# Optimization experiments

Hardware: AMD Instinct MI355X
Metric: run time of the kernel (lower is better)

Reference implementation:

```python
import jax, jax.numpy as jnp
import numpy as np

NEG_SLOPE = 0.2  # PyG GATConv default negative_slope


def gat_layer(x, edge_index, W, att_src, att_dst, bias):
    """GATConv with self-loops, concat heads. x:[N,F_in], W:[F_in,H*C]."""
    N = x.shape[0]
    H, C = att_src.shape
    loop = jnp.arange(N, dtype=edge_index.dtype)
    src = jnp.concatenate([edge_index[0], loop])  # [E+N]
    dst = jnp.concatenate([edge_index[1], loop])
    h = (x @ W).reshape(N, H, C)                  # [N,H,C]
    a_src = jnp.einsum('nhc,hc->nh', h, att_src)  # [N,H]
    a_dst = jnp.einsum('nhc,hc->nh', h, att_dst)
    e = a_src[src] + a_dst[dst]                   # [E+N,H]
    e = jnp.where(e > 0, e, NEG_SLOPE * e)        # leaky_relu
    # numerically-stable segment softmax over incoming edges of each dst node
    m = jax.ops.segment_max(e, dst, num_segments=N)           # [N,H]
    ex = jnp.exp(e - m[dst])
    denom = jax.ops.segment_sum(ex, dst, num_segments=N)      # [N,H]
    alpha = ex / (denom[dst] + 1e-16)                          # [E+N,H]
    out = jax.ops.segment_sum(h[src] * alpha[:, :, None], dst, num_segments=N)
    return out.reshape(N, H * C) + bias


def setup_inputs() -> dict:
    key = jax.random.key(0)
    ks = jax.random.split(key, 16)
    N, E, F_IN, HID, H, NCLS = 50000, 800000, 128, 64, 4, 40
    HC = H * HID
    s = 0.1
    return {
        'x': jax.random.normal(ks[0], (N, F_IN), jnp.float32),
        'edge_index': jax.random.randint(ks[1], (2, E), 0, N, jnp.int32),
        'W1': jax.random.normal(ks[2], (F_IN, HC), jnp.float32) * s,
        'att_src1': jax.random.normal(ks[3], (H, HID), jnp.float32) * s,
        'att_dst1': jax.random.normal(ks[4], (H, HID), jnp.float32) * s,
        'b1': jnp.zeros((HC,), jnp.float32),
        'W2': jax.random.normal(ks[5], (HC, HC), jnp.float32) * s,
        'att_src2': jax.random.normal(ks[6], (H, HID), jnp.float32) * s,
        'att_dst2': jax.random.normal(ks[7], (H, HID), jnp.float32) * s,
        'b2': jnp.zeros((HC,), jnp.float32),
        'fcW1': jax.random.normal(ks[8], (HC, HID), jnp.float32) * s,
        'fcb1': jnp.zeros((HID,), jnp.float32),
        'fcW2': jax.random.normal(ks[9], (HID, NCLS), jnp.float32) * s,
        'fcb2': jnp.zeros((NCLS,), jnp.float32),
    }


def reference(x, edge_index, W1, att_src1, att_dst1, b1,
              W2, att_src2, att_dst2, b2, fcW1, fcb1, fcW2, fcb2):
    h = gat_layer(x, edge_index, W1, att_src1, att_dst1, b1)
    h = jax.nn.elu(h)
    h = gat_layer(h, edge_index, W2, att_src2, att_dst2, b2)
    h = jax.nn.elu(h)
    h = jnp.maximum(h @ fcW1 + fcb1, 0.0)  # ReLU; dropout is identity in eval
    return h @ fcW2 + fcb2                 # [N, num_classes]
```

## Files before the change

kernel.cpp:

```cpp
#include <hip/hip_runtime.h>

typedef __attribute__((ext_vector_type(8))) _Float16 fp16x8;
typedef __attribute__((ext_vector_type(4))) float f32x4;
typedef __attribute__((ext_vector_type(4))) _Float16 h4;
typedef unsigned int u32;

__device__ __forceinline__ float lrelu(float x) { return x > 0.f ? x : 0.2f * x; }
__device__ __forceinline__ float elu(float x) { return x > 0.f ? x : __expf(x) - 1.f; }

__device__ __forceinline__ void gl2lds16(const void* g, void* l) {
    __builtin_amdgcn_global_load_lds((const __attribute__((address_space(1))) u32*)g,
                                     (__attribute__((address_space(3))) u32*)l, 16, 0, 0);
}

__device__ __forceinline__ void t16t_body(const float* __restrict__ W, _Float16* __restrict__ T,
                                          int N, int Nreal, int t) {
    int lane = t & 63, rem = t >> 6;
    int kk = rem & 1; rem >>= 1;
    int ncg = N / 16;
    int cg = rem % ncg, kc = rem / ncg;
    int k = kc * 64 + kk * 32 + (lane >> 4) * 8;
    int n = cg * 16 + (lane & 15);
    fp16x8 o;
#pragma unroll
    for (int j = 0; j < 8; ++j)
        o[j] = (n < Nreal) ? (_Float16)W[(size_t)(k + j) * Nreal + n] : (_Float16)0.f;
    *(fp16x8*)(T + (size_t)t * 8) = o;
}

__global__ __launch_bounds__(256) void k_prep(const float* __restrict__ W1, _Float16* __restrict__ W1T,
                                              const float* __restrict__ W2, _Float16* __restrict__ W2T,
                                              const float* __restrict__ fcW1, _Float16* __restrict__ fWT,
                                              const float* __restrict__ fcW2, _Float16* __restrict__ f2T,
                                              const int* __restrict__ dst, int* __restrict__ cnt) {
    int b = blockIdx.x, tid = threadIdx.x;
    if (b < 16)      t16t_body(W1, W1T, 256, 256, b * 256 + tid);
    else if (b < 48) t16t_body(W2, W2T, 256, 256, (b - 16) * 256 + tid);
    else if (b < 56) t16t_body(fcW1, fWT, 64, 64, (b - 48) * 256 + tid);
    else if (b < 58) t16t_body(fcW2, f2T, 64, 40, (b - 56) * 256 + tid);
    else             atomicAdd(&cnt[dst[(b - 58) * 256 + tid]], 1);
}

__global__ __launch_bounds__(256) void k_scan_a(const int* __restrict__ cnt, int* __restrict__ s,
                                                int* __restrict__ partial, int N) {
    __shared__ int sh[256];
    int t = threadIdx.x, gid = blockIdx.x * 256 + t;
    sh[t] = gid < N ? cnt[gid] : 0;
    __syncthreads();
    for (int off = 1; off < 256; off <<= 1) {
        int add = (t >= off) ? sh[t - off] : 0;
        __syncthreads();
        sh[t] += add;
        __syncthreads();
    }
    if (gid < N) s[gid] = sh[t];
    if (t == 255) partial[blockIdx.x] = sh[255];
}
__global__ __launch_bounds__(256) void k_scan_bc(const int* __restrict__ s, const int* __restrict__ partial,
                                                 const int* __restrict__ cnt, int* __restrict__ row_ptr,
                                                 int* __restrict__ cursor, int N) {
    __shared__ int red[256];
    int t = threadIdx.x, bid = blockIdx.x;
    int a = 0;
    for (int i = t; i < bid; i += 256) a += partial[i];
    red[t] = a;
    __syncthreads();
    for (int off = 128; off; off >>= 1) {
        if (t < off) red[t] += red[t + off];
        __syncthreads();
    }
    int base = red[0];
    int gid = bid * 256 + t;
    if (gid >= N) return;
    int val = s[gid] + base;
    row_ptr[gid + 1] = val;
    cursor[gid] = val - cnt[gid];
    if (gid == 0) row_ptr[0] = 0;
}

template<int KV, int NW, int ATT, int AFP32>
__device__ __forceinline__ void gemm_body(int bid,
              const _Float16* __restrict__ Ah, const float* __restrict__ Af,
              const _Float16* __restrict__ BT, _Float16* __restrict__ Chi,
              const float* __restrict__ att_s, const float* __restrict__ att_d,
              float* __restrict__ a_src, float* __restrict__ a_dst,
              int M, int Nc) {
    constexpr int NCG = NW / 16;
    constexpr int CHUNK = NW * 64;
    constexpr int FPW = (CHUNK / 512) / 4;
    __shared__ _Float16 Bs[CHUNK];
    const int m0 = bid * 64;
    const int tid = threadIdx.x;
    const int lane = tid & 63, wv = tid >> 6;
    const int r16 = lane & 15, quad = lane >> 4;
    const int arow = min(m0 + wv * 16 + r16, M - 1);

    f32x4 acc[NCG];
#pragma unroll
    for (int cg = 0; cg < NCG; ++cg) acc[cg] = (f32x4){0, 0, 0, 0};

    constexpr int NCH = KV / 64;
#pragma unroll
    for (int kc = 0; kc < NCH; ++kc) {
        if (kc) __syncthreads();
#pragma unroll
        for (int f = 0; f < FPW; ++f) {
            int fr = wv * FPW + f;
            gl2lds16(BT + (size_t)kc * CHUNK + fr * 512 + lane * 8, &Bs[fr * 512]);
        }
        fp16x8 ar[2];
        if (AFP32) {
            const float* Ap = Af + (size_t)arow * KV + kc * 64 + quad * 8;
#pragma unroll
            for (int kk = 0; kk < 2; ++kk) {
                float4 u0 = *(const float4*)(Ap + kk * 32);
                float4 u1 = *(const float4*)(Ap + kk * 32 + 4);
                fp16x8 h8;
                h8[0] = (_Float16)u0.x; h8[1] = (_Float16)u0.y;
                h8[2] = (_Float16)u0.z; h8[3] = (_Float16)u0.w;
                h8[4] = (_Float16)u1.x; h8[5] = (_Float16)u1.y;
                h8[6] = (_Float16)u1.z; h8[7] = (_Float16)u1.w;
                ar[kk] = h8;
            }
        } else {
            const _Float16* Ahp = Ah + (size_t)arow * KV + kc * 64 + quad * 8;
#pragma unroll
            for (int kk = 0; kk < 2; ++kk) ar[kk] = *(const fp16x8*)(Ahp + kk * 32);
        }
        __syncthreads();
#pragma unroll
        for (int kk = 0; kk < 2; ++kk) {
#pragma unroll
            for (int cg = 0; cg < NCG; ++cg) {
                fp16x8 bh = *(const fp16x8*)(&Bs[(cg * 2 + kk) * 512 + lane * 8]);
                acc[cg] = __builtin_amdgcn_mfma_f32_16x16x32_f16(ar[kk], bh, acc[cg], 0, 0, 0);
            }
        }
    }

    const int rbase = m0 + wv * 16 + quad * 4;

    if (ATT) {
#pragma unroll
        for (int hq = 0; hq < 4; ++hq) {
            float as[4], ad[4];
#pragma unroll
            for (int cg = 0; cg < 4; ++cg) {
                as[cg] = att_s[hq * 64 + cg * 16 + r16];
                ad[cg] = att_d[hq * 64 + cg * 16 + r16];
            }
#pragma unroll
            for (int i = 0; i < 4; ++i) {
                float ps = acc[hq * 4 + 0][i] * as[0] + acc[hq * 4 + 1][i] * as[1]
                         + acc[hq * 4 + 2][i] * as[2] + acc[hq * 4 + 3][i] * as[3];
                float pd = acc[hq * 4 + 0][i] * ad[0] + acc[hq * 4 + 1][i] * ad[1]
                         + acc[hq * 4 + 2][i] * ad[2] + acc[hq * 4 + 3][i] * ad[3];
#pragma unroll
                for (int d = 1; d < 16; d <<= 1) {
                    ps += __shfl_xor(ps, d);
                    pd += __shfl_xor(pd, d);
                }
                int r = rbase + i;
                if (r16 == 0 && r < M) {
                    a_src[(size_t)r * 4 + hq] = ps;
                    a_dst[(size_t)r * 4 + hq] = pd;
                }
            }
        }
    }

#pragma unroll
    for (int cg = 0; cg < NCG; ++cg) {
        int c = cg * 16 + r16;
        if (c >= Nc) continue;
#pragma unroll
        for (int i = 0; i < 4; ++i) {
            int r = rbase + i;
            if (r < M) Chi[(size_t)r * Nc + c] = (_Float16)acc[cg][i];
        }
    }
}

__global__ __launch_bounds__(256, 4)
void k_work1(const float* __restrict__ x, const _Float16* __restrict__ W1T,
             _Float16* __restrict__ h,
             const float* __restrict__ att_s, const float* __restrict__ att_d,
             float* __restrict__ a_src, float* __restrict__ a_dst,
             const int* __restrict__ src, const int* __restrict__ dst,
             int* __restrict__ cursor, int* __restrict__ csr,
             int M, int E, int RB) {
    if ((int)blockIdx.x >= RB) {
        int e = (blockIdx.x - RB) * 256 + threadIdx.x;
        if (e < E) {
            int d = dst[e];
            int pos = atomicAdd(&cursor[d], 1);
            csr[pos] = src[e];
        }
        return;
    }
    gemm_body<128, 256, 1, 1>(blockIdx.x, nullptr, x, W1T, h, att_s, att_d, a_src, a_dst, M, 256);
}

__global__ __launch_bounds__(256, 4)
void k_gemm2(const _Float16* __restrict__ Ah, const _Float16* __restrict__ BT,
             _Float16* __restrict__ h,
             const float* __restrict__ att_s, const float* __restrict__ att_d,
             float* __restrict__ a_src, float* __restrict__ a_dst, int M) {
    gemm_body<256, 256, 1, 0>(blockIdx.x, Ah, nullptr, BT, h, att_s, att_d, a_src, a_dst, M, 256);
}

__global__ __launch_bounds__(256, 4)
void k_fc(const _Float16* __restrict__ Ah, const _Float16* __restrict__ BT1,
          const _Float16* __restrict__ BT2, const float* __restrict__ b1,
          const float* __restrict__ b2, float* __restrict__ out, int M) {
    __shared__ _Float16 S[4096 + 64 * 72];
    const int m0 = blockIdx.x * 64;
    const int tid = threadIdx.x;
    const int lane = tid & 63, wv = tid >> 6;
    const int r16 = lane & 15, quad = lane >> 4;
    const int arow = min(m0 + wv * 16 + r16, M - 1);

    f32x4 acc[4];
#pragma unroll
    for (int cg = 0; cg < 4; ++cg) acc[cg] = (f32x4){0, 0, 0, 0};
#pragma unroll
    for (int kc = 0; kc < 4; ++kc) {
        if (kc) __syncthreads();
#pragma unroll
        for (int f = 0; f < 2; ++f) {
            int fr = wv * 2 + f;
            gl2lds16(BT1 + (size_t)kc * 4096 + fr * 512 + lane * 8, &S[fr * 512]);
        }
        fp16x8 ar[2];
        const _Float16* Ahp = Ah + (size_t)arow * 256 + kc * 64 + quad * 8;
#pragma unroll
        for (int kk = 0; kk < 2; ++kk) ar[kk] = *(const fp16x8*)(Ahp + kk * 32);
        __syncthreads();
#pragma unroll
        for (int kk = 0; kk < 2; ++kk) {
#pragma unroll
            for (int cg = 0; cg < 4; ++cg) {
                fp16x8 bh = *(const fp16x8*)(&S[(cg * 2 + kk) * 512 + lane * 8]);
                acc[cg] = __builtin_amdgcn_mfma_f32_16x16x32_f16(ar[kk], bh, acc[cg], 0, 0, 0);
            }
        }
    }
    __syncthreads();
    const int rloc = wv * 16 + quad * 4;
#pragma unroll
    for (int cg = 0; cg < 4; ++cg) {
        int c = cg * 16 + r16;
        float badd = b1[c];
#pragma unroll
        for (int i = 0; i < 4; ++i)
            S[4096 + (rloc + i) * 72 + c] = (_Float16)fmaxf(acc[cg][i] + badd, 0.f);
    }
    __syncthreads();
    const int arow2 = wv * 16 + r16;
    fp16x8 a2[2];
#pragma unroll
    for (int kk = 0; kk < 2; ++kk)
        a2[kk] = *(const fp16x8*)(&S[4096 + arow2 * 72 + kk * 32 + quad * 8]);
    f32x4 acc2[4];
#pragma unroll
    for (int cg = 0; cg < 4; ++cg) acc2[cg] = (f32x4){0, 0, 0, 0};
#pragma unroll
    for (int kk = 0; kk < 2; ++kk) {
#pragma unroll
        for (int cg = 0; cg < 4; ++cg) {
            fp16x8 bh = *(const fp16x8*)(BT2 + (cg * 2 + kk) * 512 + lane * 8);
            acc2[cg] = __builtin_amdgcn_mfma_f32_16x16x32_f16(a2[kk], bh, acc2[cg], 0, 0, 0);
        }
    }
    const int rbase = m0 + wv * 16 + quad * 4;
#pragma unroll
    for (int cg = 0; cg < 4; ++cg) {
        int c = cg * 16 + r16;
        if (c >= 40) continue;
        float badd = b2[c];
#pragma unroll
        for (int i = 0; i < 4; ++i) {
            int r = rbase + i;
            if (r < M) out[(size_t)r * 40 + c] = acc2[cg][i] + badd;
        }
    }
}

__global__ __launch_bounds__(256) void k_aggr8(const _Float16* __restrict__ h, const float* __restrict__ a_src,
                                               const float* __restrict__ a_dst, const int* __restrict__ row_ptr,
                                               const int* __restrict__ csr, const float* __restrict__ bias,
                                               _Float16* __restrict__ o_hi, int N) {
    int n = blockIdx.x * 8 + (threadIdx.x >> 5);
    if (n >= N) return;
    int cl = threadIdx.x & 31;
    int hd = cl >> 3;
    int beg = row_ptr[n], end = row_ptr[n + 1];
    float adh = a_dst[(size_t)4 * n + hd];
    const _Float16* hb = h + (size_t)cl * 8;

    float ws = __expf(lrelu(a_src[(size_t)4 * n + hd] + adh));
    fp16x8 sv = *(const fp16x8*)(hb + (size_t)n * 256);
    float acc[8];
#pragma unroll
    for (int j = 0; j < 8; ++j) acc[j] = ws * (float)sv[j];
    float dn = ws;

    int e = beg;
    for (; e + 4 <= end; e += 4) {
        int s0 = csr[e], s1 = csr[e + 1], s2 = csr[e + 2], s3 = csr[e + 3];
        float z0 = a_src[(size_t)4 * s0 + hd], z1 = a_src[(size_t)4 * s1 + hd];
        float z2 = a_src[(size_t)4 * s2 + hd], z3 = a_src[(size_t)4 * s3 + hd];
        fp16x8 v0 = *(const fp16x8*)(hb + (size_t)s0 * 256);
        fp16x8 v1 = *(const fp16x8*)(hb + (size_t)s1 * 256);
        fp16x8 v2 = *(const fp16x8*)(hb + (size_t)s2 * 256);
        fp16x8 v3 = *(const fp16x8*)(hb + (size_t)s3 * 256);
        float w0 = __expf(lrelu(z0 + adh)), w1 = __expf(lrelu(z1 + adh));
        float w2 = __expf(lrelu(z2 + adh)), w3 = __expf(lrelu(z3 + adh));
        dn += (w0 + w1) + (w2 + w3);
#pragma unroll
        for (int j = 0; j < 8; ++j)
            acc[j] += w0 * (float)v0[j] + w1 * (float)v1[j]
                    + w2 * (float)v2[j] + w3 * (float)v3[j];
    }
    for (; e + 2 <= end; e += 2) {
        int s0 = csr[e], s1 = csr[e + 1];
        float z0 = a_src[(size_t)4 * s0 + hd], z1 = a_src[(size_t)4 * s1 + hd];
        fp16x8 v0 = *(const fp16x8*)(hb + (size_t)s0 * 256);
        fp16x8 v1 = *(const fp16x8*)(hb + (size_t)s1 * 256);
        float w0 = __expf(lrelu(z0 + adh)), w1 = __expf(lrelu(z1 + adh));
        dn += w0 + w1;
#pragma unroll
        for (int j = 0; j < 8; ++j)
            acc[j] += w0 * (float)v0[j] + w1 * (float)v1[j];
    }
    if (e < end) {
        int s0 = csr[e];
        float w0 = __expf(lrelu(a_src[(size_t)4 * s0 + hd] + adh));
        fp16x8 v0 = *(const fp16x8*)(hb + (size_t)s0 * 256);
        dn += w0;
#pragma unroll
        for (int j = 0; j < 8; ++j) acc[j] += w0 * (float)v0[j];
    }

    float inv = 1.f / (dn + 1e-16f);
    float4 b0 = *(const float4*)(bias + cl * 8);
    float4 b1v = *(const float4*)(bias + cl * 8 + 4);
    fp16x8 hi;
    hi[0] = (_Float16)elu(acc[0] * inv + b0.x);
    hi[1] = (_Float16)elu(acc[1] * inv + b0.y);
    hi[2] = (_Float16)elu(acc[2] * inv + b0.z);
    hi[3] = (_Float16)elu(acc[3] * inv + b0.w);
    hi[4] = (_Float16)elu(acc[4] * inv + b1v.x);
    hi[5] = (_Float16)elu(acc[5] * inv + b1v.y);
    hi[6] = (_Float16)elu(acc[6] * inv + b1v.z);
    hi[7] = (_Float16)elu(acc[7] * inv + b1v.w);
    *(fp16x8*)(o_hi + (size_t)n * 256 + cl * 8) = hi;
}

extern "C" void kernel_launch(void* const* d_in, const int* in_sizes, int n_in,
                              void* d_out, int out_size, void* d_ws, size_t ws_size,
                              hipStream_t stream) {
    const int N = 50000, E = 800000, F_IN = 128, HC = 256, HID = 64, NCLS = 40;
    const float* x    = (const float*)d_in[0];
    const int*   ei   = (const int*)d_in[1];
    const float* W1   = (const float*)d_in[2];
    const float* as1  = (const float*)d_in[3];
    const float* ad1  = (const float*)d_in[4];
    const float* b1   = (const float*)d_in[5];
    const float* W2   = (const float*)d_in[6];
    const float* as2  = (const float*)d_in[7];
    const float* ad2  = (const float*)d_in[8];
    const float* b2   = (const float*)d_in[9];
    const float* fcW1 = (const float*)d_in[10];
    const float* fcb1 = (const float*)d_in[11];
    const float* fcW2 = (const float*)d_in[12];
    const float* fcb2 = (const float*)d_in[13];
    float* out = (float*)d_out;

    char* wp = (char*)d_ws;
    auto alloc = [&](size_t b) { char* p = wp; wp += (b + 255) & ~(size_t)255; return p; };
    _Float16* h     = (_Float16*)alloc((size_t)N * HC * 2);
    _Float16* ohi   = (_Float16*)alloc((size_t)N * HC * 2);
    float*  asrc  = (float*)alloc((size_t)N * 4 * 4);
    float*  adst  = (float*)alloc((size_t)N * 4 * 4);
    _Float16* W1T   = (_Float16*)alloc((size_t)F_IN * HC * 2);
    _Float16* W2T   = (_Float16*)alloc((size_t)HC * HC * 2);
    _Float16* fWT   = (_Float16*)alloc((size_t)HC * HID * 2);
    _Float16* f2T   = (_Float16*)alloc((size_t)HID * HID * 2);
    int* cnt     = (int*)alloc((size_t)N * 4);
    int* sbuf    = (int*)alloc((size_t)N * 4);
    int* part    = (int*)alloc(1024);
    int* row_ptr = (int*)alloc(((size_t)N + 1) * 4);
    int* cursor  = (int*)alloc((size_t)N * 4);
    int* csr     = (int*)alloc((size_t)E * 4);

    const int* src = ei;
    const int* dst = ei + E;

    const int rb = (N + 63) / 64;
    const int node_blocks8 = (N + 7) / 8;
    const int fill_blocks = (E + 255) / 256;

    hipMemsetAsync(cnt, 0, (size_t)N * 4, stream);
    k_prep<<<3183, 256, 0, stream>>>(W1, W1T, W2, W2T, fcW1, fWT, fcW2, f2T, dst, cnt);
    int nb = (N + 255) / 256;
    k_scan_a<<<nb, 256, 0, stream>>>(cnt, sbuf, part, N);
    k_scan_bc<<<nb, 256, 0, stream>>>(sbuf, part, cnt, row_ptr, cursor, N);
    k_work1<<<rb + fill_blocks, 256, 0, stream>>>(x, W1T, h, as1, ad1, asrc, adst,
                                                  src, dst, cursor, csr, N, E, rb);
    k_aggr8<<<node_blocks8, 256, 0, stream>>>(h, asrc, adst, row_ptr, csr, b1, ohi, N);
    k_gemm2<<<rb, 256, 0, stream>>>(ohi, W2T, h, as2, ad2, asrc, adst, N);
    k_aggr8<<<node_blocks8, 256, 0, stream>>>(h, asrc, adst, row_ptr, csr, b2, ohi, N);
    k_fc<<<rb, 256, 0, stream>>>(ohi, fWT, f2T, fcb1, fcb2, out, N);
}
```

Measured before the change: 351.6 us.

## Split GAT aggregation into attention-weight pass and column-sliced aggregation

```diff
diff --git a/kernel.cpp b/kernel.cpp
--- a/kernel.cpp
+++ b/kernel.cpp
@@ -286,75 +286,102 @@
     }
 }
 
-__global__ __launch_bounds__(256) void k_aggr8(const _Float16* __restrict__ h, const float* __restrict__ a_src,
-                                               const float* __restrict__ a_dst, const int* __restrict__ row_ptr,
-                                               const int* __restrict__ csr, const float* __restrict__ bias,
-                                               _Float16* __restrict__ o_hi, int N) {
-    int n = blockIdx.x * 8 + (threadIdx.x >> 5);
+__global__ __launch_bounds__(256) void k_attw(const float* __restrict__ a_src,
+        const float* __restrict__ a_dst, const int* __restrict__ row_ptr,
+        const int* __restrict__ csr, float* __restrict__ w,
+        float* __restrict__ invdn, float* __restrict__ wself, int N, int E) {
+    int t = blockIdx.x * 256 + threadIdx.x;
+    int n = t >> 2, hd = t & 3;
     if (n >= N) return;
-    int cl = threadIdx.x & 31;
-    int hd = cl >> 3;
     int beg = row_ptr[n], end = row_ptr[n + 1];
-    float adh = a_dst[(size_t)4 * n + hd];
-    const _Float16* hb = h + (size_t)cl * 8;
-
-    float ws = __expf(lrelu(a_src[(size_t)4 * n + hd] + adh));
-    fp16x8 sv = *(const fp16x8*)(hb + (size_t)n * 256);
-    float acc[8];
-#pragma unroll
-    for (int j = 0; j < 8; ++j) acc[j] = ws * (float)sv[j];
+    float ad = a_dst[(size_t)n * 4 + hd];
+    float ws = __expf(lrelu(a_src[(size_t)n * 4 + hd] + ad));
     float dn = ws;
-
+    float* wh = w + (size_t)hd * E;
     int e = beg;
-    for (; e + 4 <= end; e += 4) {
-        int s0 = csr[e], s1 = csr[e + 1], s2 = csr[e + 2], s3 = csr[e + 3];
-        float z0 = a_src[(size_t)4 * s0 + hd], z1 = a_src[(size_t)4 * s1 + hd];
-        float z2 = a_src[(size_t)4 * s2 + hd], z3 = a_src[(size_t)4 * s3 + hd];
-        fp16x8 v0 = *(const fp16x8*)(hb + (size_t)s0 * 256);
-        fp16x8 v1 = *(const fp16x8*)(hb + (size_t)s1 * 256);
-        fp16x8 v2 = *(const fp16x8*)(hb + (size_t)s2 * 256);
-        fp16x8 v3 = *(const fp16x8*)(hb + (size_t)s3 * 256);
-        float w0 = __expf(lrelu(z0 + adh)), w1 = __expf(lrelu(z1 + adh));
-        float w2 = __expf(lrelu(z2 + adh)), w3 = __expf(lrelu(z3 + adh));
-        dn += (w0 + w1) + (w2 + w3);
-#pragma unroll
-        for (int j = 0; j < 8; ++j)
-            acc[j] += w0 * (float)v0[j] + w1 * (float)v1[j]
-                    + w2 * (float)v2[j] + w3 * (float)v3[j];
-    }
     for (; e + 2 <= end; e += 2) {
         int s0 = csr[e], s1 = csr[e + 1];
-        float z0 = a_src[(size_t)4 * s0 + hd], z1 = a_src[(size_t)4 * s1 + hd];
-        fp16x8 v0 = *(const fp16x8*)(hb + (size_t)s0 * 256);
-        fp16x8 v1 = *(const fp16x8*)(hb + (size_t)s1 * 256);
-        float w0 = __expf(lrelu(z0 + adh)), w1 = __expf(lrelu(z1 + adh));
+        float z0 = a_src[(size_t)s0 * 4 + hd];
+        float z1 = a_src[(size_t)s1 * 4 + hd];
+        float w0 = __expf(lrelu(z0 + ad));
+        float w1 = __expf(lrelu(z1 + ad));
+        wh[e] = w0; wh[e + 1] = w1;
         dn += w0 + w1;
-#pragma unroll
-        for (int j = 0; j < 8; ++j)
-            acc[j] += w0 * (float)v0[j] + w1 * (float)v1[j];
     }
     if (e < end) {
         int s0 = csr[e];
-        float w0 = __expf(lrelu(a_src[(size_t)4 * s0 + hd] + adh));
-        fp16x8 v0 = *(const fp16x8*)(hb + (size_t)s0 * 256);
+        float w0 = __expf(lrelu(a_src[(size_t)s0 * 4 + hd] + ad));
+        wh[e] = w0;
         dn += w0;
-#pragma unroll
-        for (int j = 0; j < 8; ++j) acc[j] += w0 * (float)v0[j];
-    }
-
-    float inv = 1.f / (dn + 1e-16f);
-    float4 b0 = *(const float4*)(bias + cl * 8);
-    float4 b1v = *(const float4*)(bias + cl * 8 + 4);
-    fp16x8 hi;
-    hi[0] = (_Float16)elu(acc[0] * inv + b0.x);
-    hi[1] = (_Float16)elu(acc[1] * inv + b0.y);
-    hi[2] = (_Float16)elu(acc[2] * inv + b0.z);
-    hi[3] = (_Float16)elu(acc[3] * inv + b0.w);
-    hi[4] = (_Float16)elu(acc[4] * inv + b1v.x);
-    hi[5] = (_Float16)elu(acc[5] * inv + b1v.y);
-    hi[6] = (_Float16)elu(acc[6] * inv + b1v.z);
-    hi[7] = (_Float16)elu(acc[7] * inv + b1v.w);
-    *(fp16x8*)(o_hi + (size_t)n * 256 + cl * 8) = hi;
+    }
+    wself[(size_t)n * 4 + hd] = ws;
+    invdn[(size_t)n * 4 + hd] = 1.f / (dn + 1e-16f);
+}
+
+#define AGGR_CPN 196
+__global__ __launch_bounds__(256, 8) void k_aggr9(const _Float16* __restrict__ h,
+        const float* __restrict__ w, const float* __restrict__ invdn,
+        const float* __restrict__ wself, const int* __restrict__ row_ptr,
+        const int* __restrict__ csr, const float* __restrict__ bias,
+        _Float16* __restrict__ o, int N, int E) {
+    const int bid = blockIdx.x;
+    const int s = bid & 7, chunk = bid >> 3;
+    const int gi = threadIdx.x >> 2, L = threadIdx.x & 3;
+    const int hd = s >> 1;
+    const _Float16* hb = h + s * 32 + L * 8;
+    const float* wh = w + (size_t)hd * E;
+    const int cbase = chunk * AGGR_CPN;
+    float bv[8];
+    {
+        float4 b0 = *(const float4*)(bias + s * 32 + L * 8);
+        float4 b1v = *(const float4*)(bias + s * 32 + L * 8 + 4);
+        bv[0] = b0.x; bv[1] = b0.y; bv[2] = b0.z; bv[3] = b0.w;
+        bv[4] = b1v.x; bv[5] = b1v.y; bv[6] = b1v.z; bv[7] = b1v.w;
+    }
+#pragma unroll 1
+    for (int k = 0; k < 4; ++k) {
+        int r = k * 64 + gi;
+        if (r >= AGGR_CPN) break;
+        int n = cbase + r;
+        if (n >= N) break;
+        int beg = row_ptr[n], end = row_ptr[n + 1];
+        float wsf = wself[(size_t)n * 4 + hd];
+        float inv = invdn[(size_t)n * 4 + hd];
+        fp16x8 sv = *(const fp16x8*)(hb + (size_t)n * 256);
+        float acc[8];
+#pragma unroll
+        for (int j = 0; j < 8; ++j) acc[j] = wsf * (float)sv[j];
+        int e = beg;
+        for (; e + 4 <= end; e += 4) {
+            int s0 = __builtin_nontemporal_load(csr + e);
+            int s1 = __builtin_nontemporal_load(csr + e + 1);
+            int s2 = __builtin_nontemporal_load(csr + e + 2);
+            int s3 = __builtin_nontemporal_load(csr + e + 3);
+            float w0 = __builtin_nontemporal_load(wh + e);
+            float w1 = __builtin_nontemporal_load(wh + e + 1);
+            float w2 = __builtin_nontemporal_load(wh + e + 2);
+            float w3 = __builtin_nontemporal_load(wh + e + 3);
+            fp16x8 v0 = *(const fp16x8*)(hb + (size_t)s0 * 256);
+            fp16x8 v1 = *(const fp16x8*)(hb + (size_t)s1 * 256);
+            fp16x8 v2 = *(const fp16x8*)(hb + (size_t)s2 * 256);
+            fp16x8 v3 = *(const fp16x8*)(hb + (size_t)s3 * 256);
+#pragma unroll
+            for (int j = 0; j < 8; ++j)
+                acc[j] += w0 * (float)v0[j] + w1 * (float)v1[j]
+                        + w2 * (float)v2[j] + w3 * (float)v3[j];
+        }
+        for (; e < end; ++e) {
+            int s0 = csr[e];
+            float w0 = wh[e];
+            fp16x8 v0 = *(const fp16x8*)(hb + (size_t)s0 * 256);
+#pragma unroll
+            for (int j = 0; j < 8; ++j) acc[j] += w0 * (float)v0[j];
+        }
+        fp16x8 hi;
+#pragma unroll
+        for (int j = 0; j < 8; ++j) hi[j] = (_Float16)elu(acc[j] * inv + bv[j]);
+        __builtin_nontemporal_store(hi, (fp16x8*)(o + (size_t)n * 256 + s * 32 + L * 8));
+    }
 }
 
 extern "C" void kernel_launch(void* const* d_in, const int* in_sizes, int n_in,
@@ -393,13 +420,17 @@
     int* row_ptr = (int*)alloc(((size_t)N + 1) * 4);
     int* cursor  = (int*)alloc((size_t)N * 4);
     int* csr     = (int*)alloc((size_t)E * 4);
+    float* w4    = (float*)alloc((size_t)E * 4 * 4);
+    float* invd  = (float*)alloc((size_t)N * 4 * 4);
+    float* wslf  = (float*)alloc((size_t)N * 4 * 4);
 
     const int* src = ei;
     const int* dst = ei + E;
 
     const int rb = (N + 63) / 64;
-    const int node_blocks8 = (N + 7) / 8;
     const int fill_blocks = (E + 255) / 256;
+    const int attw_blocks = (N * 4 + 255) / 256;
+    const int aggr_blocks = 8 * ((N + AGGR_CPN - 1) / AGGR_CPN);
 
     hipMemsetAsync(cnt, 0, (size_t)N * 4, stream);
     k_prep<<<3183, 256, 0, stream>>>(W1, W1T, W2, W2T, fcW1, fWT, fcW2, f2T, dst, cnt);
@@ -408,8 +439,10 @@
     k_scan_bc<<<nb, 256, 0, stream>>>(sbuf, part, cnt, row_ptr, cursor, N);
     k_work1<<<rb + fill_blocks, 256, 0, stream>>>(x, W1T, h, as1, ad1, asrc, adst,
                                                   src, dst, cursor, csr, N, E, rb);
-    k_aggr8<<<node_blocks8, 256, 0, stream>>>(h, asrc, adst, row_ptr, csr, b1, ohi, N);
+    k_attw<<<attw_blocks, 256, 0, stream>>>(asrc, adst, row_ptr, csr, w4, invd, wslf, N, E);
+    k_aggr9<<<aggr_blocks, 256, 0, stream>>>(h, w4, invd, wslf, row_ptr, csr, b1, ohi, N, E);
     k_gemm2<<<rb, 256, 0, stream>>>(ohi, W2T, h, as2, ad2, asrc, adst, N);
-    k_aggr8<<<node_blocks8, 256, 0, stream>>>(h, asrc, adst, row_ptr, csr, b2, ohi, N);
+    k_attw<<<attw_blocks, 256, 0, stream>>>(asrc, adst, row_ptr, csr, w4, invd, wslf, N, E);
+    k_aggr9<<<aggr_blocks, 256, 0, stream>>>(h, w4, invd, wslf, row_ptr, csr, b2, ohi, N, E);
     k_fc<<<rb, 256, 0, stream>>>(ohi, fWT, f2T, fcb1, fcb2, out, N);
 }
```

Measured after the change: 555.8 us. +58.1%, slower.

## Pre-bin edges by destination range before CSR fill for locality

Applied to the files above, without the earlier changes.

```diff
diff --git a/kernel.cpp b/kernel.cpp
--- a/kernel.cpp
+++ b/kernel.cpp
@@ -58,7 +58,7 @@
 }
 __global__ __launch_bounds__(256) void k_scan_bc(const int* __restrict__ s, const int* __restrict__ partial,
                                                  const int* __restrict__ cnt, int* __restrict__ row_ptr,
-                                                 int* __restrict__ cursor, int N) {
+                                                 int* __restrict__ cursor, int* __restrict__ bcur, int N) {
     __shared__ int red[256];
     int t = threadIdx.x, bid = blockIdx.x;
     int a = 0;
@@ -74,8 +74,62 @@
     if (gid >= N) return;
     int val = s[gid] + base;
     row_ptr[gid + 1] = val;
-    cursor[gid] = val - cnt[gid];
+    int excl = val - cnt[gid];
+    cursor[gid] = excl;
+    if ((gid & 511) == 0) bcur[gid >> 9] = excl;
     if (gid == 0) row_ptr[0] = 0;
+}
+
+__global__ __launch_bounds__(256) void k_bin(const int* __restrict__ src, const int* __restrict__ dst,
+                                             int* __restrict__ bcur, int2* __restrict__ pairbuf, int E) {
+    __shared__ int cnt[128], gbase[128], excl[128], cur2[128], sh[128];
+    __shared__ int saddr[1024];
+    __shared__ int2 spair[1024];
+    const int tid = threadIdx.x;
+    const int eb = blockIdx.x * 1024;
+    if (tid < 128) { cnt[tid] = 0; cur2[tid] = 0; }
+    __syncthreads();
+    int s_[4], d_[4];
+#pragma unroll
+    for (int j = 0; j < 4; ++j) {
+        int e = eb + j * 256 + tid;
+        if (e < E) {
+            s_[j] = src[e]; d_[j] = dst[e];
+            atomicAdd(&cnt[d_[j] >> 9], 1);
+        } else d_[j] = -1;
+    }
+    __syncthreads();
+    if (tid < 128) sh[tid] = cnt[tid];
+    __syncthreads();
+    for (int off = 1; off < 128; off <<= 1) {
+        int add = 0;
+        if (tid < 128 && tid >= off) add = sh[tid - off];
+        __syncthreads();
+        if (tid < 128) sh[tid] += add;
+        __syncthreads();
+    }
+    if (tid < 128) {
+        excl[tid] = sh[tid] - cnt[tid];
+        if (cnt[tid] > 0) gbase[tid] = atomicAdd(&bcur[tid], cnt[tid]);
+    }
+    __syncthreads();
+#pragma unroll
+    for (int j = 0; j < 4; ++j) {
+        if (d_[j] >= 0) {
+            int b = d_[j] >> 9;
+            int r = atomicAdd(&cur2[b], 1);
+            int slot = excl[b] + r;
+            spair[slot] = make_int2(s_[j], d_[j]);
+            saddr[slot] = gbase[b] + r;
+        }
+    }
+    __syncthreads();
+    int tot = min(1024, E - eb);
+#pragma unroll
+    for (int j = 0; j < 4; ++j) {
+        int slot = j * 256 + tid;
+        if (slot < tot) pairbuf[saddr[slot]] = spair[slot];
+    }
 }
 
 template<int KV, int NW, int ATT, int AFP32>
@@ -186,15 +240,19 @@
              _Float16* __restrict__ h,
              const float* __restrict__ att_s, const float* __restrict__ att_d,
              float* __restrict__ a_src, float* __restrict__ a_dst,
-             const int* __restrict__ src, const int* __restrict__ dst,
+             const int2* __restrict__ pairbuf,
              int* __restrict__ cursor, int* __restrict__ csr,
              int M, int E, int RB) {
     if ((int)blockIdx.x >= RB) {
-        int e = (blockIdx.x - RB) * 256 + threadIdx.x;
-        if (e < E) {
-            int d = dst[e];
-            int pos = atomicAdd(&cursor[d], 1);
-            csr[pos] = src[e];
+        int base = (blockIdx.x - RB) * 1024;
+#pragma unroll
+        for (int j = 0; j < 4; ++j) {
+            int i = base + j * 256 + threadIdx.x;
+            if (i < E) {
+                int2 p = pairbuf[i];
+                int pos = atomicAdd(&cursor[p.y], 1);
+                csr[pos] = p.x;
+            }
         }
         return;
     }
@@ -393,21 +451,25 @@
     int* row_ptr = (int*)alloc(((size_t)N + 1) * 4);
     int* cursor  = (int*)alloc((size_t)N * 4);
     int* csr     = (int*)alloc((size_t)E * 4);
+    int* bcur    = (int*)alloc(128 * 4);
+    int2* pairs  = (int2*)alloc((size_t)E * 8);
 
     const int* src = ei;
     const int* dst = ei + E;
 
     const int rb = (N + 63) / 64;
     const int node_blocks8 = (N + 7) / 8;
-    const int fill_blocks = (E + 255) / 256;
+    const int bin_blocks = (E + 1023) / 1024;
+    const int p2_blocks = (E + 1023) / 1024;
 
     hipMemsetAsync(cnt, 0, (size_t)N * 4, stream);
     k_prep<<<3183, 256, 0, stream>>>(W1, W1T, W2, W2T, fcW1, fWT, fcW2, f2T, dst, cnt);
     int nb = (N + 255) / 256;
     k_scan_a<<<nb, 256, 0, stream>>>(cnt, sbuf, part, N);
-    k_scan_bc<<<nb, 256, 0, stream>>>(sbuf, part, cnt, row_ptr, cursor, N);
-    k_work1<<<rb + fill_blocks, 256, 0, stream>>>(x, W1T, h, as1, ad1, asrc, adst,
-                                                  src, dst, cursor, csr, N, E, rb);
+    k_scan_bc<<<nb, 256, 0, stream>>>(sbuf, part, cnt, row_ptr, cursor, bcur, N);
+    k_bin<<<bin_blocks, 256, 0, stream>>>(src, dst, bcur, pairs, E);
+    k_work1<<<rb + p2_blocks, 256, 0, stream>>>(x, W1T, h, as1, ad1, asrc, adst,
+                                                pairs, cursor, csr, N, E, rb);
     k_aggr8<<<node_blocks8, 256, 0, stream>>>(h, asrc, adst, row_ptr, csr, b1, ohi, N);
     k_gemm2<<<rb, 256, 0, stream>>>(ohi, W2T, h, as2, ad2, asrc, adst, N);
     k_aggr8<<<node_blocks8, 256, 0, stream>>>(h, asrc, adst, row_ptr, csr, b2, ohi, N);
```

Result: faster. 340.0 us (-3.3%).
